# Optimization experiments

Hardware: AMD Instinct MI355X
Metric: run time of the kernel (lower is better)

Reference implementation:

```python
import jax, jax.numpy as jnp
import numpy as np

B, H, W, C = 8, 112, 112, 128
NH, WS, SR, HIDDEN = 4, 7, 8, 512
EPS = 1e-5

def ln(x, g, b):
    mu = jnp.mean(x, axis=-1, keepdims=True)
    var = jnp.var(x, axis=-1, keepdims=True)
    return (x - mu) * jax.lax.rsqrt(var + EPS) * g + b

def local_attn(x, qkv_w, qkv_b, pw, pb):
    # windowed attention: (H,W) tiled into WSxWS windows, H%WS==W%WS==0 so no pad
    Bx, N, Cx = x.shape
    hd = Cx // NH
    _h, _w = H // WS, W // WS
    xw = x.reshape(Bx, _h, WS, _w, WS, Cx).transpose(0, 1, 3, 2, 4, 5)
    xw = xw.reshape(Bx, _h * _w, WS * WS, Cx)
    qkv = (xw @ qkv_w + qkv_b).reshape(Bx, _h * _w, WS * WS, 3, NH, hd)
    qkv = qkv.transpose(3, 0, 1, 4, 2, 5)  # 3, B, nW, NH, ws2, hd
    q, k, v = qkv[0], qkv[1], qkv[2]
    attn = jax.nn.softmax((q @ jnp.swapaxes(k, -2, -1)) * (hd ** -0.5), axis=-1)
    o = (attn @ v).transpose(0, 1, 3, 2, 4).reshape(Bx, _h, _w, WS, WS, Cx)
    o = o.transpose(0, 1, 3, 2, 4, 5).reshape(Bx, N, Cx)
    return o @ pw + pb

def global_attn(x, qw, qb, kvw, kvb, srw, srb, sng, snb, pw, pb):
    Bx, N, Cx = x.shape
    hd = Cx // NH
    q = (x @ qw + qb).reshape(Bx, N, NH, hd).transpose(0, 2, 1, 3)  # B,NH,N,hd
    xi = x.reshape(Bx, H, W, Cx)
    xs = jax.lax.conv_general_dilated(xi, srw, (SR, SR), 'VALID',
                                      dimension_numbers=('NHWC', 'HWIO', 'NHWC')) + srb
    xs = ln(xs.reshape(Bx, -1, Cx), sng, snb)  # B, M, C  (M = (H/SR)*(W/SR))
    kv = (xs @ kvw + kvb).reshape(Bx, -1, 2, NH, hd)
    k = kv[:, :, 0].transpose(0, 2, 1, 3)
    v = kv[:, :, 1].transpose(0, 2, 1, 3)
    attn = jax.nn.softmax(jnp.einsum('bhnd,bhmd->bhnm', q, k) * (hd ** -0.5), axis=-1)
    o = jnp.einsum('bhnm,bhmd->bhnd', attn, v).transpose(0, 2, 1, 3).reshape(Bx, N, Cx)
    return o @ pw + pb

def mlp(x, f1w, f1b, dww, dwb, f2w, f2b):
    h = x @ f1w + f1b
    hi = h.reshape(x.shape[0], H, W, HIDDEN)
    hi = jax.lax.conv_general_dilated(hi, dww, (1, 1), 'SAME',
                                      dimension_numbers=('NHWC', 'HWIO', 'NHWC'),
                                      feature_group_count=HIDDEN) + dwb
    h = jax.nn.gelu(hi.reshape(x.shape[0], -1, HIDDEN), approximate=False)
    return h @ f2w + f2b

def reference(x, l_n1_g, l_n1_b, l_qkv_w, l_qkv_b, l_pw, l_pb, l_n2_g, l_n2_b,
              l_f1w, l_f1b, l_dww, l_dwb, l_f2w, l_f2b,
              g_n1_g, g_n1_b, g_qw, g_qb, g_kvw, g_kvb, g_srw, g_srb, g_sng, g_snb,
              g_pw, g_pb, g_n2_g, g_n2_b, g_f1w, g_f1b, g_dww, g_dwb, g_f2w, g_f2b):
    # Local-attention Block
    x = x + local_attn(ln(x, l_n1_g, l_n1_b), l_qkv_w, l_qkv_b, l_pw, l_pb)
    x = x + mlp(ln(x, l_n2_g, l_n2_b), l_f1w, l_f1b, l_dww, l_dwb, l_f2w, l_f2b)
    # Global (spatial-reduction) attention Block
    x = x + global_attn(ln(x, g_n1_g, g_n1_b), g_qw, g_qb, g_kvw, g_kvb,
                        g_srw, g_srb, g_sng, g_snb, g_pw, g_pb)
    x = x + mlp(ln(x, g_n2_g, g_n2_b), g_f1w, g_f1b, g_dww, g_dwb, g_f2w, g_f2b)
    return x

def setup_inputs() -> dict:
    key = jax.random.key(0)
    cnt = [0]
    def rn(shp, s=0.02):
        cnt[0] += 1
        return (jax.random.normal(jax.random.fold_in(key, cnt[0]), shp, dtype=jnp.float32) * s)
    z = lambda shp: jnp.zeros(shp, jnp.float32)
    o = lambda shp: jnp.ones(shp, jnp.float32)
    return {
        'x': rn((B, H * W, C), 1.0),
        'l_n1_g': o((C,)), 'l_n1_b': z((C,)),
        'l_qkv_w': rn((C, 3 * C)), 'l_qkv_b': z((3 * C,)),
        'l_pw': rn((C, C)), 'l_pb': z((C,)),
        'l_n2_g': o((C,)), 'l_n2_b': z((C,)),
        'l_f1w': rn((C, HIDDEN)), 'l_f1b': z((HIDDEN,)),
        'l_dww': rn((3, 3, 1, HIDDEN), 0.1), 'l_dwb': z((HIDDEN,)),
        'l_f2w': rn((HIDDEN, C)), 'l_f2b': z((C,)),
        'g_n1_g': o((C,)), 'g_n1_b': z((C,)),
        'g_qw': rn((C, C)), 'g_qb': z((C,)),
        'g_kvw': rn((C, 2 * C)), 'g_kvb': z((2 * C,)),
        'g_srw': rn((SR, SR, C, C), 0.02), 'g_srb': z((C,)),
        'g_sng': o((C,)), 'g_snb': z((C,)),
        'g_pw': rn((C, C)), 'g_pb': z((C,)),
        'g_n2_g': o((C,)), 'g_n2_b': z((C,)),
        'g_f1w': rn((C, HIDDEN)), 'g_f1b': z((HIDDEN,)),
        'g_dww': rn((3, 3, 1, HIDDEN), 0.1), 'g_dwb': z((HIDDEN,)),
        'g_f2w': rn((HIDDEN, C)), 'g_f2b': z((C,)),
    }
```

## Files before the change

kernel.cpp:

```cpp
#include <hip/hip_runtime.h>
#include <hip/hip_bf16.h>

#define DI __device__ __forceinline__

typedef __attribute__((ext_vector_type(8))) __bf16 bf16x8;
typedef __attribute__((ext_vector_type(8))) short short8;
typedef __attribute__((ext_vector_type(4))) short short4v;
typedef __attribute__((ext_vector_type(4))) float f32x4;
typedef __attribute__((ext_vector_type(2))) float f32x2;

DI short f2b(float f) {
    union { float f; unsigned u; } v; v.f = f;
    unsigned r = v.u + 0x7FFFu + ((v.u >> 16) & 1u);
    return (short)(r >> 16);
}
DI float b2f(short s) {
    union { unsigned u; float f; } v; v.u = ((unsigned)(unsigned short)s) << 16;
    return v.f;
}
DI float lo16(int x) {
    union { unsigned u; float f; } v; v.u = (unsigned)x << 16; return v.f;
}
DI float hi16(int x) {
    union { unsigned u; float f; } v; v.u = (unsigned)x & 0xffff0000u; return v.f;
}

DI void gll16(const short* g, short* l) {
    __builtin_amdgcn_global_load_lds(
        (const __attribute__((address_space(1))) void*)(g),
        (__attribute__((address_space(3))) void*)(l), 16, 0, 0);
}

DI float gelu(float a) {
    float t = __expf(-1.702f * a);
    return a * __builtin_amdgcn_rcpf(1.f + t);
}

template<int OB, int HB, int HR, int LNO, int FULLK>
__global__ __launch_bounds__(512)
void gemm128(const short* __restrict__ A, int lda,
             const short* __restrict__ Wt, int ldw,
             const float* __restrict__ bias,
             void* __restrict__ Cv, int ldc,
             const short* __restrict__ R, int ldr,
             const float* __restrict__ lng, const float* __restrict__ lnb,
             short* __restrict__ lnout,
             int K)
{
    __shared__ short As[16384];
    __shared__ short Bs[16384];
    const int nx = gridDim.x;
    const int total = nx * gridDim.y;
    int bid = blockIdx.x + nx * blockIdx.y;
    if ((total & 7) == 0) bid = (bid & 7) * (total >> 3) + (bid >> 3);
    const int m0 = (bid / nx) * 128, n0 = (bid % nx) * 128;
    const int tid = threadIdx.x, lane = tid & 63, w = tid >> 6;
    const int wr = w >> 2, wc = w & 3;
    const int fr = lane & 15, fg = lane >> 4;
    const int mB = wr * 64 + fr;
    const int nB = wc * 32 + fg * 4;
    const int x7 = fr & 7;

    int2 rpre[4][2];
    if (HR) {
        #pragma unroll
        for (int mi = 0; mi < 4; mi++) {
            const long long m = m0 + mB + mi * 16;
            #pragma unroll
            for (int ni = 0; ni < 2; ni++)
                rpre[mi][ni] = *(const int2*)&R[m * ldr + n0 + nB + ni * 16];
        }
    }

    f32x4 zero = {0.f, 0.f, 0.f, 0.f};
    f32x4 acc[4][2];
    #pragma unroll
    for (int i = 0; i < 4; i++)
        #pragma unroll
        for (int j = 0; j < 2; j++) acc[i][j] = zero;

    if (FULLK) {
        #pragma unroll
        for (int i = 0; i < 4; i++) {
            const int row = i * 32 + w * 4 + (lane >> 4);
            const int chunk = lane & 15;
            const int scol = (chunk ^ (row & 7)) * 8;
            short* dA = As + (i * 32 + w * 4) * 128 + lane * 8;
            short* dB = Bs + (i * 32 + w * 4) * 128 + lane * 8;
            gll16(A  + (long long)(m0 + row) * lda + scol, dA);
            gll16(Wt + (long long)(n0 + row) * ldw + scol, dB);
        }
        asm volatile("s_waitcnt vmcnt(0)" ::: "memory");
        __builtin_amdgcn_s_barrier();
        __builtin_amdgcn_s_setprio(1);
        #pragma unroll
        for (int kt = 0; kt < 4; kt++) {
            const int kc = ((kt * 4 + fg) ^ x7) * 8;
            bf16x8 af[4], bfr[2];
            #pragma unroll
            for (int mi = 0; mi < 4; mi++)
                af[mi] = *(const bf16x8*)(As + (mB + mi * 16) * 128 + kc);
            #pragma unroll
            for (int ni = 0; ni < 2; ni++)
                bfr[ni] = *(const bf16x8*)(Bs + (wc * 32 + ni * 16 + fr) * 128 + kc);
            #pragma unroll
            for (int mi = 0; mi < 4; mi++)
                #pragma unroll
                for (int ni = 0; ni < 2; ni++)
                    acc[mi][ni] = __builtin_amdgcn_mfma_f32_16x16x32_bf16(bfr[ni], af[mi], acc[mi][ni], 0, 0, 0);
        }
        __builtin_amdgcn_s_setprio(0);
    } else {
        auto STAGE = [&](int buf, int t) {
            #pragma unroll
            for (int i = 0; i < 2; i++) {
                const int row = i * 64 + w * 8 + (lane >> 3);
                const int chunk = lane & 7;
                const int scol = t * 64 + (chunk ^ (row & 7)) * 8;
                short* dA = As + buf * 8192 + (i * 64 + w * 8) * 64 + lane * 8;
                short* dB = Bs + buf * 8192 + (i * 64 + w * 8) * 64 + lane * 8;
                gll16(A  + (long long)(m0 + row) * lda + scol, dA);
                gll16(Wt + (long long)(n0 + row) * ldw + scol, dB);
            }
        };
        auto COMPUTE = [&](int buf) {
            __builtin_amdgcn_s_setprio(1);
            #pragma unroll
            for (int kt = 0; kt < 2; kt++) {
                const int kc = ((kt * 4 + fg) ^ x7) * 8;
                bf16x8 af[4], bfr[2];
                #pragma unroll
                for (int mi = 0; mi < 4; mi++)
                    af[mi] = *(const bf16x8*)(As + buf * 8192 + (mB + mi * 16) * 64 + kc);
                #pragma unroll
                for (int ni = 0; ni < 2; ni++)
                    bfr[ni] = *(const bf16x8*)(Bs + buf * 8192 + (wc * 32 + ni * 16 + fr) * 64 + kc);
                #pragma unroll
                for (int mi = 0; mi < 4; mi++)
                    #pragma unroll
                    for (int ni = 0; ni < 2; ni++)
                        acc[mi][ni] = __builtin_amdgcn_mfma_f32_16x16x32_bf16(bfr[ni], af[mi], acc[mi][ni], 0, 0, 0);
            }
            __builtin_amdgcn_s_setprio(0);
        };
        const int NT = K >> 6;
        STAGE(0, 0);
        for (int t = 0; t < NT; t++) {
            if (t + 1 < NT) {
                STAGE((t + 1) & 1, t + 1);
                asm volatile("s_waitcnt vmcnt(4)" ::: "memory");
            } else {
                asm volatile("s_waitcnt vmcnt(0)" ::: "memory");
            }
            __builtin_amdgcn_s_barrier();
            COMPUTE(t & 1);
            __builtin_amdgcn_s_barrier();
        }
    }

    if (LNO) {
        float s1[4] = {0.f, 0.f, 0.f, 0.f}, s2[4] = {0.f, 0.f, 0.f, 0.f};
        #pragma unroll
        for (int mi = 0; mi < 4; mi++) {
            const long long m = m0 + mB + mi * 16;
            #pragma unroll
            for (int ni = 0; ni < 2; ni++) {
                const int n = nB + ni * 16;
                float4 bv = *(const float4*)&bias[n];
                const float* bvp = (const float*)&bv;
                float rv[4] = {lo16(rpre[mi][ni].x), hi16(rpre[mi][ni].x),
                               lo16(rpre[mi][ni].y), hi16(rpre[mi][ni].y)};
                #pragma unroll
                for (int v = 0; v < 4; v++) {
                    float val = acc[mi][ni][v] + bvp[v] + rv[v];
                    acc[mi][ni][v] = val;
                    s1[mi] += val;
                    s2[mi] += val * val;
                }
                int2 pk;
                pk.x = ((int)(unsigned short)f2b(acc[mi][ni][1]) << 16) | (unsigned short)f2b(acc[mi][ni][0]);
                pk.y = ((int)(unsigned short)f2b(acc[mi][ni][3]) << 16) | (unsigned short)f2b(acc[mi][ni][2]);
                *(int2*)&((short*)Cv)[m * ldc + n] = pk;
            }
        }
        #pragma unroll
        for (int mi = 0; mi < 4; mi++) {
            s1[mi] += __shfl_xor(s1[mi], 16); s1[mi] += __shfl_xor(s1[mi], 32);
            s2[mi] += __shfl_xor(s2[mi], 16); s2[mi] += __shfl_xor(s2[mi], 32);
        }
        float* sc = (float*)As;
        __syncthreads();
        if (fg == 0) {
            #pragma unroll
            for (int mi = 0; mi < 4; mi++) {
                int rt = mB + mi * 16;
                sc[rt * 8 + wc * 2]     = s1[mi];
                sc[rt * 8 + wc * 2 + 1] = s2[mi];
            }
        }
        __syncthreads();
        #pragma unroll
        for (int mi = 0; mi < 4; mi++) {
            int rt = mB + mi * 16;
            long long m = m0 + rt;
            float t1 = (sc[rt * 8 + 0] + sc[rt * 8 + 2]) + (sc[rt * 8 + 4] + sc[rt * 8 + 6]);
            float t2 = (sc[rt * 8 + 1] + sc[rt * 8 + 3]) + (sc[rt * 8 + 5] + sc[rt * 8 + 7]);
            float mu = t1 * 0.0078125f;
            float var = t2 * 0.0078125f - mu * mu;
            float rs = rsqrtf(var + 1e-5f);
            #pragma unroll
            for (int ni = 0; ni < 2; ni++) {
                int n = nB + ni * 16;
                float4 gg = *(const float4*)&lng[n];
                float4 bb = *(const float4*)&lnb[n];
                const float* gp = (const float*)&gg;
                const float* bp = (const float*)&bb;
                short o[4];
                #pragma unroll
                for (int v = 0; v < 4; v++)
                    o[v] = f2b((acc[mi][ni][v] - mu) * rs * gp[v] + bp[v]);
                int2 pk;
                pk.x = ((int)(unsigned short)o[1] << 16) | (unsigned short)o[0];
                pk.y = ((int)(unsigned short)o[3] << 16) | (unsigned short)o[2];
                *(int2*)&lnout[m * 128 + n] = pk;
            }
        }
    } else {
        #pragma unroll
        for (int mi = 0; mi < 4; mi++) {
            const long long m = m0 + mB + mi * 16;
            #pragma unroll
            for (int ni = 0; ni < 2; ni++) {
                const int n = n0 + nB + ni * 16;
                float4 bv = {0.f, 0.f, 0.f, 0.f};
                if (HB) bv = *(const float4*)&bias[n];
                const float* bvp = (const float*)&bv;
                float rv[4] = {0.f, 0.f, 0.f, 0.f};
                if (HR) {
                    rv[0] = lo16(rpre[mi][ni].x); rv[1] = hi16(rpre[mi][ni].x);
                    rv[2] = lo16(rpre[mi][ni].y); rv[3] = hi16(rpre[mi][ni].y);
                }
                float val[4];
                #pragma unroll
                for (int v = 0; v < 4; v++)
                    val[v] = acc[mi][ni][v] + bvp[v] + rv[v];
                if (OB) {
                    int2 pk;
                    pk.x = ((int)(unsigned short)f2b(val[1]) << 16) | (unsigned short)f2b(val[0]);
                    pk.y = ((int)(unsigned short)f2b(val[3]) << 16) | (unsigned short)f2b(val[2]);
                    *(int2*)&((short*)Cv)[m * ldc + n] = pk;
                } else {
                    float4 st = {val[0], val[1], val[2], val[3]};
                    *(float4*)&((float*)Cv)[m * ldc + n] = st;
                }
            }
        }
    }
}

template<int OB, int HB>
__global__ __launch_bounds__(256)
void gemm64(const short* __restrict__ A, int lda, long long sA,
            const short* __restrict__ Wt, int ldw, long long sW,
            const float* __restrict__ bias,
            void* __restrict__ Cv, int ldc, long long sC,
            int M, int N, int K)
{
    __shared__ short As[2048];
    __shared__ short Bs[2048];
    const int z = blockIdx.z;
    A  += (long long)z * sA;
    Wt += (long long)z * sW;
    const int m0 = blockIdx.y * 64, n0 = blockIdx.x * 64;
    const int tid = threadIdx.x, lane = tid & 63, wv = tid >> 6;
    const int wr = wv >> 1, wc = wv & 1;
    const int lrow = tid >> 2, lch = tid & 3;
    const int wch = lch ^ (lrow & 3);

    f32x4 zero = {0.f, 0.f, 0.f, 0.f};
    f32x4 acc00 = zero, acc01 = zero, acc10 = zero, acc11 = zero;

    const short* arow = &A[(long long)(m0 + lrow) * lda + lch * 8];
    const short* brow = &Wt[(long long)(n0 + lrow) * ldw + lch * 8];
    short* asw = &As[lrow * 32 + wch * 8];
    short* bsw = &Bs[lrow * 32 + wch * 8];

    const int fr = lane & 15, fg = lane >> 4;
    const int c = ((fg ^ (fr & 3)) * 8);
    const int a0off = (wr * 32 + fr) * 32 + c;
    const int b0off = (wc * 32 + fr) * 32 + c;

    for (int k0 = 0; k0 < K; k0 += 32) {
        uint4 av = *(const uint4*)arow; arow += 32;
        uint4 bv = *(const uint4*)brow; brow += 32;
        __syncthreads();
        *(uint4*)asw = av;
        *(uint4*)bsw = bv;
        __syncthreads();
        bf16x8 a0 = *(const bf16x8*)&As[a0off];
        bf16x8 a1 = *(const bf16x8*)&As[a0off + 512];
        bf16x8 b0 = *(const bf16x8*)&Bs[b0off];
        bf16x8 b1 = *(const bf16x8*)&Bs[b0off + 512];
        acc00 = __builtin_amdgcn_mfma_f32_16x16x32_bf16(a0, b0, acc00, 0, 0, 0);
        acc01 = __builtin_amdgcn_mfma_f32_16x16x32_bf16(a0, b1, acc01, 0, 0, 0);
        acc10 = __builtin_amdgcn_mfma_f32_16x16x32_bf16(a1, b0, acc10, 0, 0, 0);
        acc11 = __builtin_amdgcn_mfma_f32_16x16x32_bf16(a1, b1, acc11, 0, 0, 0);
    }

    const long long cz = (long long)z * sC;
    const int rbase = m0 + wr * 32 + fg * 4;
    const int cbase = n0 + wc * 32 + fr;
    auto emit = [&](f32x4 a, int mi, int ni) {
        int cc = cbase + ni * 16;
        if (cc >= N) return;
        float bv = HB ? bias[cc] : 0.f;
        #pragma unroll
        for (int v = 0; v < 4; v++) {
            int rr = rbase + mi * 16 + v;
            if (rr >= M) continue;
            float val = a[v] + bv;
            if (OB) ((short*)Cv)[cz + (long long)rr * ldc + cc] = f2b(val);
            else    ((float*)Cv)[cz + (long long)rr * ldc + cc] = val;
        }
    };
    emit(acc00, 0, 0); emit(acc01, 0, 1); emit(acc10, 1, 0); emit(acc11, 1, 1);
}

__global__ __launch_bounds__(256)
void srgemm(const short* __restrict__ LNF, const short* __restrict__ Wt,
            float* __restrict__ PART)
{
    __shared__ short As[2048];
    __shared__ short Bs[2048];
    const int z = blockIdx.z;
    const int m0 = blockIdx.y * 64, n0 = blockIdx.x * 64;
    const int tid = threadIdx.x, lane = tid & 63, wv = tid >> 6;
    const int wr = wv >> 1, wc = wv & 1;
    const int lrow = tid >> 2, lch = tid & 3;
    const int wch = lch ^ (lrow & 3);

    f32x4 zero = {0.f, 0.f, 0.f, 0.f};
    f32x4 acc00 = zero, acc01 = zero, acc10 = zero, acc11 = zero;

    int row = m0 + lrow;
    int rc = row < 1568 ? row : 1567;
    int b = rc / 196, p = rc % 196;
    int oh = p / 14, ow = p % 14;
    int k0 = z * 256;
    int kh = k0 >> 10, koff = k0 & 1023;
    const short* arow = LNF + ((long long)(b * 12544 + (oh * 8 + kh) * 112 + ow * 8)) * 128
                        + koff + lch * 8;
    const short* brow = Wt + (long long)(n0 + lrow) * 8192 + k0 + lch * 8;
    short* asw = &As[lrow * 32 + wch * 8];
    short* bsw = &Bs[lrow * 32 + wch * 8];

    const int fr = lane & 15, fg = lane >> 4;
    const int c = ((fg ^ (fr & 3)) * 8);
    const int a0off = (wr * 32 + fr) * 32 + c;
    const int b0off = (wc * 32 + fr) * 32 + c;

    for (int kk = 0; kk < 256; kk += 32) {
        uint4 av = *(const uint4*)arow; arow += 32;
        uint4 bv = *(const uint4*)brow; brow += 32;
        __syncthreads();
        *(uint4*)asw = av;
        *(uint4*)bsw = bv;
        __syncthreads();
        bf16x8 a0 = *(const bf16x8*)&As[a0off];
        bf16x8 a1 = *(const bf16x8*)&As[a0off + 512];
        bf16x8 b0 = *(const bf16x8*)&Bs[b0off];
        bf16x8 b1 = *(const bf16x8*)&Bs[b0off + 512];
        acc00 = __builtin_amdgcn_mfma_f32_16x16x32_bf16(a0, b0, acc00, 0, 0, 0);
        acc01 = __builtin_amdgcn_mfma_f32_16x16x32_bf16(a0, b1, acc01, 0, 0, 0);
        acc10 = __builtin_amdgcn_mfma_f32_16x16x32_bf16(a1, b0, acc10, 0, 0, 0);
        acc11 = __builtin_amdgcn_mfma_f32_16x16x32_bf16(a1, b1, acc11, 0, 0, 0);
    }

    const int rbase = m0 + wr * 32 + fg * 4;
    const int cbase = n0 + wc * 32 + fr;
    auto emit = [&](f32x4 a, int mi, int ni) {
        int cc = cbase + ni * 16;
        #pragma unroll
        for (int v = 0; v < 4; v++) {
            int rr = rbase + mi * 16 + v;
            if (rr >= 1568) continue;
            PART[(long long)z * 200704 + (long long)rr * 128 + cc] = a[v];
        }
    };
    emit(acc00, 0, 0); emit(acc01, 0, 1); emit(acc10, 1, 0); emit(acc11, 1, 1);
}

__global__ void reduceXS(const float* __restrict__ PART, const float* __restrict__ bias,
                         float* __restrict__ XS)
{
    int i = blockIdx.x * 256 + threadIdx.x;
    float s = 0.f;
    #pragma unroll
    for (int z = 0; z < 32; z++) s += PART[(long long)z * 200704 + i];
    XS[i] = s + bias[i & 127];
}

__global__ __launch_bounds__(256)
void ln_kernel(const float* __restrict__ x, const float* __restrict__ g,
               const float* __restrict__ b, short* __restrict__ o, int rows)
{
    int row = blockIdx.x * 4 + (threadIdx.x >> 6);
    if (row >= rows) return;
    int lane = threadIdx.x & 63;
    const float2 v = *(const float2*)&x[(long long)row * 128 + lane * 2];
    float s = v.x + v.y;
    float ss = v.x * v.x + v.y * v.y;
    #pragma unroll
    for (int off = 1; off < 64; off <<= 1) {
        s += __shfl_xor(s, off);
        ss += __shfl_xor(ss, off);
    }
    float mu = s * 0.0078125f;
    float var = ss * 0.0078125f - mu * mu;
    float rs = rsqrtf(var + 1e-5f);
    float2 gg = *(const float2*)&g[lane * 2];
    float2 bb = *(const float2*)&b[lane * 2];
    short2 out;
    out.x = f2b((v.x - mu) * rs * gg.x + bb.x);
    out.y = f2b((v.y - mu) * rs * gg.y + bb.y);
    *(short2*)&o[(long long)row * 128 + lane * 2] = out;
}

__global__ __launch_bounds__(256)
void ln_first(const float* __restrict__ x, const float* __restrict__ g,
              const float* __restrict__ b, short* __restrict__ o,
              short* __restrict__ res)
{
    int row = blockIdx.x * 4 + (threadIdx.x >> 6);
    int lane = threadIdx.x & 63;
    const float2 v = *(const float2*)&x[(long long)row * 128 + lane * 2];
    short2 rc;
    rc.x = f2b(v.x); rc.y = f2b(v.y);
    *(short2*)&res[(long long)row * 128 + lane * 2] = rc;
    float s = v.x + v.y;
    float ss = v.x * v.x + v.y * v.y;
    #pragma unroll
    for (int off = 1; off < 64; off <<= 1) {
        s += __shfl_xor(s, off);
        ss += __shfl_xor(ss, off);
    }
    float mu = s * 0.0078125f;
    float var = ss * 0.0078125f - mu * mu;
    float rs = rsqrtf(var + 1e-5f);
    float2 gg = *(const float2*)&g[lane * 2];
    float2 bb = *(const float2*)&b[lane * 2];
    short2 out;
    out.x = f2b((v.x - mu) * rs * gg.x + bb.x);
    out.y = f2b((v.y - mu) * rs * gg.y + bb.y);
    *(short2*)&o[(long long)row * 128 + lane * 2] = out;
}

__global__ void wtrans(const float* __restrict__ w, short* __restrict__ wt, int K, int N)
{
    long long idx = (long long)blockIdx.x * 256 + threadIdx.x;
    if (idx >= (long long)K * N) return;
    int k = (int)(idx / N), n = (int)(idx % N);
    wt[(long long)n * K + k] = f2b(w[idx]);
}

__global__ void packkv(const short* __restrict__ kvb, short* __restrict__ kp,
                       short* __restrict__ vt)
{
    int idx = blockIdx.x * 256 + threadIdx.x;
    if (idx >= 229376) return;
    int d = idx & 31;
    int m = (idx >> 5) % 224;
    int bh = idx / (224 * 32);
    int b = bh >> 2, h = bh & 3;
    short kv = 0, vv = 0;
    if (m < 196) {
        long long src = ((long long)b * 196 + m) * 256 + h * 32 + d;
        kv = kvb[src];
        vv = kvb[src + 128];
    }
    if (m < 208) kp[((long long)bh * 208 + m) * 32 + d] = kv;
    vt[((long long)bh * 32 + d) * 224 + m] = vv;
}

__global__ __launch_bounds__(512)
void lattn(const short* __restrict__ qkv, short* __restrict__ att)
{
    __shared__ short QKs[64 * 264];
    __shared__ short Vt[128 * 72];
    __shared__ short Pl[8 * 16 * 72];
    const int bi = blockIdx.x >> 8;
    const int win = blockIdx.x & 255;
    const int wy = win >> 4, wx = win & 15;
    const long long base = (long long)bi * 12544;
    const int tid = threadIdx.x;

    for (int i = tid; i < 1152; i += 512) {
        uint4 zz = {0, 0, 0, 0};
        *(uint4*)&Vt[i * 8] = zz;
    }
    __syncthreads();

    for (int idx = tid; idx < 2352; idx += 512) {
        int i = idx / 48, ch = idx % 48;
        long long n = base + (wy * 7 + i / 7) * 112 + wx * 7 + i % 7;
        uint4 v = *(const uint4*)&qkv[n * 384 + ch * 8];
        if (ch < 32) {
            *(uint4*)&QKs[i * 264 + ch * 8] = v;
        } else {
            int c0 = (ch - 32) * 8;
            const short* sp = (const short*)&v;
            #pragma unroll
            for (int u = 0; u < 8; u++) {
                int cc = c0 + u;
                Vt[cc * 72 + ((((i >> 3) ^ ((cc >> 3) & 7)) << 3) | (i & 7))] = sp[u];
            }
        }
    }
    __syncthreads();

    const int w = tid >> 6, l = tid & 63;
    const int h = w >> 1, qh = w & 1;
    const int q16 = l & 15, g = l >> 4;
    const float SC = 0.17677669529663689f;
    f32x4 zero = {0.f, 0.f, 0.f, 0.f};

    bf16x8 kf[4];
    #pragma unroll
    for (int kt = 0; kt < 4; kt++)
        kf[kt] = *(const bf16x8*)&QKs[(kt * 16 + q16) * 264 + 128 + h * 32 + g * 8];
    bf16x8 vf[2][2];
    #pragma unroll
    for (int dt = 0; dt < 2; dt++) {
        int cc = h * 32 + dt * 16 + q16;
        #pragma unroll
        for (int s2 = 0; s2 < 2; s2++)
            vf[dt][s2] = *(const bf16x8*)&Vt[cc * 72 + (((s2 * 4 + g) ^ ((cc >> 3) & 7)) << 3)];
    }
    short* pw = &Pl[(w * 16 + q16) * 72];

    for (int qt2 = 0; qt2 < 2; qt2++) {
        int qt = qh * 2 + qt2;
        bf16x8 qf = *(const bf16x8*)&QKs[(qt * 16 + q16) * 264 + h * 32 + g * 8];
        f32x4 s[4];
        #pragma unroll
        for (int kt = 0; kt < 4; kt++)
            s[kt] = __builtin_amdgcn_mfma_f32_16x16x32_bf16(kf[kt], qf, zero, 0, 0, 0);
        float mx = -1e30f;
        #pragma unroll
        for (int kt = 0; kt < 4; kt++) {
            #pragma unroll
            for (int v = 0; v < 4; v++) {
                int k = kt * 16 + g * 4 + v;
                if (k < 49) mx = fmaxf(mx, s[kt][v]);
            }
        }
        mx = fmaxf(mx, __shfl_xor(mx, 16));
        mx = fmaxf(mx, __shfl_xor(mx, 32));
        float sum = 0.f;
        #pragma unroll
        for (int kt = 0; kt < 4; kt++) {
            #pragma unroll
            for (int v = 0; v < 4; v++) {
                int k = kt * 16 + g * 4 + v;
                float p = (k < 49) ? __expf(SC * (s[kt][v] - mx)) : 0.f;
                s[kt][v] = p;
                sum += p;
            }
        }
        sum += __shfl_xor(sum, 16);
        sum += __shfl_xor(sum, 32);
        float inv = 1.f / sum;
        #pragma unroll
        for (int kt = 0; kt < 4; kt++) {
            int lo = ((int)(unsigned short)f2b(s[kt][1] * inv) << 16) | (unsigned short)f2b(s[kt][0] * inv);
            int hi = ((int)(unsigned short)f2b(s[kt][3] * inv) << 16) | (unsigned short)f2b(s[kt][2] * inv);
            int2 pr; pr.x = lo; pr.y = hi;
            *(int2*)&pw[kt * 16 + g * 4] = pr;
        }
        f32x4 o0 = zero, o1 = zero;
        #pragma unroll
        for (int s2 = 0; s2 < 2; s2++) {
            bf16x8 pa = *(const bf16x8*)&pw[s2 * 32 + g * 8];
            o0 = __builtin_amdgcn_mfma_f32_16x16x32_bf16(pa, vf[0][s2], o0, 0, 0, 0);
            o1 = __builtin_amdgcn_mfma_f32_16x16x32_bf16(pa, vf[1][s2], o1, 0, 0, 0);
        }
        #pragma unroll
        for (int v = 0; v < 4; v++) {
            int q = qt * 16 + g * 4 + v;
            if (q < 49) {
                long long n = base + (wy * 7 + q / 7) * 112 + wx * 7 + q % 7;
                att[n * 128 + h * 32 + q16]      = f2b(o0[v]);
                att[n * 128 + h * 32 + 16 + q16] = f2b(o1[v]);
            }
        }
    }
}

__global__ __launch_bounds__(256)
void gattn(const short* __restrict__ Q, const short* __restrict__ KP,
           const short* __restrict__ VT, short* __restrict__ O)
{
    __shared__ short Ks[208 * 40];
    __shared__ short Vt[32 * 232];
    __shared__ short Pl[4 * 16 * 136];
    const int qb = blockIdx.x;
    const int bh = blockIdx.y;
    const int b = bh >> 2, h = bh & 3;
    const int tid = threadIdx.x, w = tid >> 6, l = tid & 63;
    const int q16 = l & 15, g = l >> 4;

    for (int idx = tid; idx < 832; idx += 256) {
        int m = idx >> 2, dg = idx & 3;
        uint4 v = *(const uint4*)&KP[((long long)bh * 208 + m) * 32 + dg * 8];
        *(uint4*)&Ks[m * 40 + ((dg ^ (m & 3)) * 8)] = v;
    }
    for (int idx = tid; idx < 896; idx += 256) {
        int d = idx / 28, mg = idx % 28;
        uint4 v = *(const uint4*)&VT[((long long)bh * 32 + d) * 224 + mg * 8];
        *(uint4*)&Vt[d * 232 + mg * 8] = v;
    }
    const long long qbase = (long long)b * 12544 + qb * 128 + w * 32;
    bf16x8 qfa = *(const bf16x8*)&Q[(qbase + q16) * 128 + h * 32 + g * 8];
    bf16x8 qfb = *(const bf16x8*)&Q[(qbase + 16 + q16) * 128 + h * 32 + g * 8];
    __syncthreads();

    const float SC = 0.17677669529663689f;
    f32x4 zero = {0.f, 0.f, 0.f, 0.f};
    short* pw = &Pl[(w * 16 + q16) * 136];
    const int xk = (g ^ (q16 & 3)) * 8;

    #pragma unroll
    for (int qt = 0; qt < 2; qt++) {
        bf16x8 qf = qt ? qfb : qfa;
        f32x4 s[13];
        #pragma unroll
        for (int t = 0; t < 13; t++) {
            bf16x8 a = *(const bf16x8*)&Ks[(t * 16 + q16) * 40 + xk];
            s[t] = __builtin_amdgcn_mfma_f32_16x16x32_bf16(a, qf, zero, 0, 0, 0);
        }
        float sum = 0.f;
        #pragma unroll
        for (int t = 0; t < 8; t++) {
            float p0 = __expf(SC * s[t][0]);
            float p1 = __expf(SC * s[t][1]);
            float p2 = __expf(SC * s[t][2]);
            float p3 = __expf(SC * s[t][3]);
            sum += (p0 + p1) + (p2 + p3);
            int2 pr;
            pr.x = ((int)(unsigned short)f2b(p1) << 16) | (unsigned short)f2b(p0);
            pr.y = ((int)(unsigned short)f2b(p3) << 16) | (unsigned short)f2b(p2);
            *(int2*)&pw[t * 16 + g * 4] = pr;
        }
        f32x4 o0 = zero, o1 = zero;
        #pragma unroll
        for (int kc = 0; kc < 4; kc++) {
            bf16x8 pa = *(const bf16x8*)&pw[kc * 32 + g * 8];
            bf16x8 v0 = *(const bf16x8*)&Vt[q16 * 232 + kc * 32 + g * 8];
            bf16x8 v1 = *(const bf16x8*)&Vt[(16 + q16) * 232 + kc * 32 + g * 8];
            o0 = __builtin_amdgcn_mfma_f32_16x16x32_bf16(v0, pa, o0, 0, 0, 0);
            o1 = __builtin_amdgcn_mfma_f32_16x16x32_bf16(v1, pa, o1, 0, 0, 0);
        }
        #pragma unroll
        for (int t = 8; t < 13; t++) {
            float p[4];
            #pragma unroll
            for (int v = 0; v < 4; v++) {
                int k = t * 16 + g * 4 + v;
                p[v] = (k < 196) ? __expf(SC * s[t][v]) : 0.f;
                sum += p[v];
            }
            int2 pr;
            pr.x = ((int)(unsigned short)f2b(p[1]) << 16) | (unsigned short)f2b(p[0]);
            pr.y = ((int)(unsigned short)f2b(p[3]) << 16) | (unsigned short)f2b(p[2]);
            *(int2*)&pw[(t - 8) * 16 + g * 4] = pr;
        }
        {
            int2 zz; zz.x = 0; zz.y = 0;
            *(int2*)&pw[80 + g * 4] = zz;
        }
        sum += __shfl_xor(sum, 16);
        sum += __shfl_xor(sum, 32);
        #pragma unroll
        for (int kc = 0; kc < 3; kc++) {
            bf16x8 pa = *(const bf16x8*)&pw[kc * 32 + g * 8];
            bf16x8 v0 = *(const bf16x8*)&Vt[q16 * 232 + 128 + kc * 32 + g * 8];
            bf16x8 v1 = *(const bf16x8*)&Vt[(16 + q16) * 232 + 128 + kc * 32 + g * 8];
            o0 = __builtin_amdgcn_mfma_f32_16x16x32_bf16(v0, pa, o0, 0, 0, 0);
            o1 = __builtin_amdgcn_mfma_f32_16x16x32_bf16(v1, pa, o1, 0, 0, 0);
        }
        const float inv = 1.f / sum;
        const long long r = qbase + qt * 16 + q16;
        int2 p0, p1;
        p0.x = ((int)(unsigned short)f2b(o0[1] * inv) << 16) | (unsigned short)f2b(o0[0] * inv);
        p0.y = ((int)(unsigned short)f2b(o0[3] * inv) << 16) | (unsigned short)f2b(o0[2] * inv);
        p1.x = ((int)(unsigned short)f2b(o1[1] * inv) << 16) | (unsigned short)f2b(o1[0] * inv);
        p1.y = ((int)(unsigned short)f2b(o1[3] * inv) << 16) | (unsigned short)f2b(o1[2] * inv);
        *(int2*)&O[r * 128 + h * 32 + g * 4]      = p0;
        *(int2*)&O[r * 128 + h * 32 + 16 + g * 4] = p1;
    }
}

__global__ __launch_bounds__(256)
void dwgelu(const short* __restrict__ h1, const float* __restrict__ w,
            const float* __restrict__ bias, short* __restrict__ h2)
{
    int bid = blockIdx.x;
    bid = (bid & 7) * (gridDim.x >> 3) + (bid >> 3);
    const int idx = bid * 256 + threadIdx.x;
    const int cg = idx & 127;
    const int rem = idx >> 7;
    const int img = rem / 1568;
    const int t = rem % 1568;
    const int x0 = (t % 56) * 2;
    const int y0 = (t / 56) * 4;
    const int c0 = cg << 2;

    f32x2 wreg[9][2];
    #pragma unroll
    for (int tp = 0; tp < 9; tp++) {
        float4 v = *(const float4*)&w[tp * 512 + c0];
        wreg[tp][0][0] = v.x; wreg[tp][0][1] = v.y;
        wreg[tp][1][0] = v.z; wreg[tp][1][1] = v.w;
    }
    float4 bv = *(const float4*)&bias[c0];
    f32x2 acc[4][2][2];
    #pragma unroll
    for (int r = 0; r < 4; r++)
        #pragma unroll
        for (int oc = 0; oc < 2; oc++) {
            acc[r][oc][0][0] = bv.x; acc[r][oc][0][1] = bv.y;
            acc[r][oc][1][0] = bv.z; acc[r][oc][1][1] = bv.w;
        }
    const long long ibase = (long long)img * 12544;

    if (x0 >= 1 && x0 <= 109 && y0 >= 1 && y0 <= 107) {
        const short* base = &h1[(ibase + (long long)(y0 - 1) * 112 + (x0 - 1)) * 512 + c0];
        #pragma unroll
        for (int dy = 0; dy < 6; dy++) {
            f32x2 rowf[4][2];
            #pragma unroll
            for (int kx = 0; kx < 4; kx++) {
                short4v sv = *(const short4v*)&base[((long long)dy * 112 + kx) * 512];
                rowf[kx][0][0] = b2f(sv[0]); rowf[kx][0][1] = b2f(sv[1]);
                rowf[kx][1][0] = b2f(sv[2]); rowf[kx][1][1] = b2f(sv[3]);
            }
            #pragma unroll
            for (int ky = 0; ky < 3; ky++) {
                const int r = dy - ky;
                if (r < 0 || r > 3) continue;
                #pragma unroll
                for (int oc = 0; oc < 2; oc++)
                    #pragma unroll
                    for (int kx = 0; kx < 3; kx++) {
                        acc[r][oc][0] = __builtin_elementwise_fma(rowf[oc + kx][0], wreg[ky * 3 + kx][0], acc[r][oc][0]);
                        acc[r][oc][1] = __builtin_elementwise_fma(rowf[oc + kx][1], wreg[ky * 3 + kx][1], acc[r][oc][1]);
                    }
            }
        }
    } else {
        #pragma unroll
        for (int dy = -1; dy <= 4; dy++) {
            const int yy = y0 + dy;
            const bool rowok = (unsigned)yy < 112u;
            f32x2 rowf[4][2];
            #pragma unroll
            for (int kx = 0; kx < 4; kx++) {
                const int xx = x0 - 1 + kx;
                short4v sv = {0, 0, 0, 0};
                if (rowok && (unsigned)xx < 112u)
                    sv = *(const short4v*)&h1[(ibase + yy * 112 + xx) * 512 + c0];
                rowf[kx][0][0] = b2f(sv[0]); rowf[kx][0][1] = b2f(sv[1]);
                rowf[kx][1][0] = b2f(sv[2]); rowf[kx][1][1] = b2f(sv[3]);
            }
            #pragma unroll
            for (int ky = 0; ky < 3; ky++) {
                const int r = dy + 1 - ky;
                if (r < 0 || r > 3) continue;
                #pragma unroll
                for (int oc = 0; oc < 2; oc++)
                    #pragma unroll
                    for (int kx = 0; kx < 3; kx++) {
                        acc[r][oc][0] = __builtin_elementwise_fma(rowf[oc + kx][0], wreg[ky * 3 + kx][0], acc[r][oc][0]);
                        acc[r][oc][1] = __builtin_elementwise_fma(rowf[oc + kx][1], wreg[ky * 3 + kx][1], acc[r][oc][1]);
                    }
            }
        }
    }
    #pragma unroll
    for (int r = 0; r < 4; r++)
        #pragma unroll
        for (int oc = 0; oc < 2; oc++) {
            short o[4];
            o[0] = f2b(gelu(acc[r][oc][0][0]));
            o[1] = f2b(gelu(acc[r][oc][0][1]));
            o[2] = f2b(gelu(acc[r][oc][1][0]));
            o[3] = f2b(gelu(acc[r][oc][1][1]));
            int2 pk;
            pk.x = ((int)(unsigned short)o[1] << 16) | (unsigned short)o[0];
            pk.y = ((int)(unsigned short)o[3] << 16) | (unsigned short)o[2];
            *(int2*)&h2[(ibase + (y0 + r) * 112 + x0 + oc) * 512 + c0] = pk;
        }
}

extern "C" void kernel_launch(void* const* d_in, const int* in_sizes, int n_in,
                              void* d_out, int out_size, void* d_ws, size_t ws_size,
                              hipStream_t stream)
{
    (void)in_sizes; (void)n_in; (void)out_size;
    const float* X      = (const float*)d_in[0];
    const float* l_n1_g = (const float*)d_in[1];
    const float* l_n1_b = (const float*)d_in[2];
    const float* l_qkv_w= (const float*)d_in[3];
    const float* l_qkv_b= (const float*)d_in[4];
    const float* l_pw   = (const float*)d_in[5];
    const float* l_pb   = (const float*)d_in[6];
    const float* l_n2_g = (const float*)d_in[7];
    const float* l_n2_b = (const float*)d_in[8];
    const float* l_f1w  = (const float*)d_in[9];
    const float* l_f1b  = (const float*)d_in[10];
    const float* l_dww  = (const float*)d_in[11];
    const float* l_dwb  = (const float*)d_in[12];
    const float* l_f2w  = (const float*)d_in[13];
    const float* l_f2b  = (const float*)d_in[14];
    const float* g_n1_g = (const float*)d_in[15];
    const float* g_n1_b = (const float*)d_in[16];
    const float* g_qw   = (const float*)d_in[17];
    const float* g_qb   = (const float*)d_in[18];
    const float* g_kvw  = (const float*)d_in[19];
    const float* g_kvb  = (const float*)d_in[20];
    const float* g_srw  = (const float*)d_in[21];
    const float* g_srb  = (const float*)d_in[22];
    const float* g_sng  = (const float*)d_in[23];
    const float* g_snb  = (const float*)d_in[24];
    const float* g_pw   = (const float*)d_in[25];
    const float* g_pb   = (const float*)d_in[26];
    const float* g_n2_g = (const float*)d_in[27];
    const float* g_n2_b = (const float*)d_in[28];
    const float* g_f1w  = (const float*)d_in[29];
    const float* g_f1b  = (const float*)d_in[30];
    const float* g_dww  = (const float*)d_in[31];
    const float* g_dwb  = (const float*)d_in[32];
    const float* g_f2w  = (const float*)d_in[33];
    const float* g_f2b  = (const float*)d_in[34];

    const long long NPB = 12544;
    const long long BN  = 100352;

    float* OUT = (float*)d_out;
    char* ws = (char*)d_ws;
    size_t off = 0;
    auto alloc = [&](size_t bytes) { size_t o = off; off += (bytes + 255) & ~(size_t)255; return o; };
    short* WT_QKV = (short*)(ws + alloc(384 * 128 * 2));
    short* WT_LPW = (short*)(ws + alloc(128 * 128 * 2));
    short* WT_LF1 = (short*)(ws + alloc(512 * 128 * 2));
    short* WT_LF2 = (short*)(ws + alloc(128 * 512 * 2));
    short* WT_GQ  = (short*)(ws + alloc(128 * 128 * 2));
    short* WT_GKV = (short*)(ws + alloc(256 * 128 * 2));
    short* WT_GSR = (short*)(ws + alloc(128 * 8192 * 2));
    short* WT_GPW = (short*)(ws + alloc(128 * 128 * 2));
    short* WT_GF1 = (short*)(ws + alloc(512 * 128 * 2));
    short* WT_GF2 = (short*)(ws + alloc(128 * 512 * 2));
    short* LNF    = (short*)(ws + alloc((size_t)BN * 128 * 2));
    short* RES    = (short*)(ws + alloc((size_t)BN * 128 * 2));
    char*  U      = ws + alloc(0);

    const size_t SZ_H1   = (size_t)BN * 512 * 2;
    const bool big = ws_size >= off + 2 * SZ_H1 + 4096;
    short* QKVB = (short*)(U + 0);
    short* ATT  = (short*)(U + 77070336);
    float* PART = (float*)(U + 0);
    float* XS   = (float*)(U + 25690368);
    short* XSLN = (short*)(U + 26493184);
    short* KVB  = (short*)(U + 26894592);
    short* QBUF = (short*)(U + 27697408);
    short* KP   = (short*)(U + 53387776);
    short* VT   = (short*)(U + 53387776 + 425984);

    wtrans<<<192, 256, 0, stream>>>(l_qkv_w, WT_QKV, 128, 384);
    wtrans<<<64, 256, 0, stream>>>(l_pw, WT_LPW, 128, 128);
    wtrans<<<256, 256, 0, stream>>>(l_f1w, WT_LF1, 128, 512);
    wtrans<<<256, 256, 0, stream>>>(l_f2w, WT_LF2, 512, 128);
    wtrans<<<64, 256, 0, stream>>>(g_qw, WT_GQ, 128, 128);
    wtrans<<<128, 256, 0, stream>>>(g_kvw, WT_GKV, 128, 256);
    wtrans<<<4096, 256, 0, stream>>>(g_srw, WT_GSR, 8192, 128);
    wtrans<<<64, 256, 0, stream>>>(g_pw, WT_GPW, 128, 128);
    wtrans<<<256, 256, 0, stream>>>(g_f1w, WT_GF1, 128, 512);
    wtrans<<<256, 256, 0, stream>>>(g_f2w, WT_GF2, 512, 128);

    const int CB = big ? 8 : 2;
    short* H1 = (short*)(U + 0);

    ln_first<<<25088, 256, 0, stream>>>(X, l_n1_g, l_n1_b, LNF, RES);
    gemm128<1, 1, 0, 0, 1><<<dim3(3, 784), 512, 0, stream>>>(
        LNF, 128, WT_QKV, 128, l_qkv_b, QKVB, 384, nullptr, 0,
        nullptr, nullptr, nullptr, 128);
    lattn<<<2048, 512, 0, stream>>>(QKVB, ATT);
    gemm128<1, 1, 1, 1, 1><<<dim3(1, 784), 512, 0, stream>>>(
        ATT, 128, WT_LPW, 128, l_pb, RES, 128, RES, 128,
        l_n2_g, l_n2_b, LNF, 128);

    {
        short* H2 = (short*)(U + (size_t)CB * NPB * 512 * 2);
        for (int b0 = 0; b0 < 8; b0 += CB) {
            int Mc = CB * 12544;
            gemm128<1, 1, 0, 0, 1><<<dim3(4, Mc / 128), 512, 0, stream>>>(
                LNF + (long long)b0 * NPB * 128, 128, WT_LF1, 128, l_f1b,
                H1, 512, nullptr, 0, nullptr, nullptr, nullptr, 128);
            dwgelu<<<CB * 784, 256, 0, stream>>>(H1, l_dww, l_dwb, H2);
            gemm128<1, 1, 1, 1, 0><<<dim3(1, Mc / 128), 512, 0, stream>>>(
                H2, 512, WT_LF2, 512, l_f2b,
                RES + (long long)b0 * NPB * 128, 128,
                RES + (long long)b0 * NPB * 128, 128,
                g_n1_g, g_n1_b, LNF + (long long)b0 * NPB * 128, 512);
        }
    }

    gemm128<1, 1, 0, 0, 1><<<dim3(1, 784), 512, 0, stream>>>(
        LNF, 128, WT_GQ, 128, g_qb, QBUF, 128, nullptr, 0,
        nullptr, nullptr, nullptr, 128);
    srgemm<<<dim3(2, 25, 32), 256, 0, stream>>>(LNF, WT_GSR, PART);
    reduceXS<<<784, 256, 0, stream>>>(PART, g_srb, XS);
    ln_kernel<<<392, 256, 0, stream>>>(XS, g_sng, g_snb, XSLN, 1568);
    gemm64<1, 1><<<dim3(4, 25, 1), 256, 0, stream>>>(
        XSLN, 128, 0, WT_GKV, 128, 0, g_kvb,
        KVB, 256, 0, 1568, 256, 128);
    packkv<<<896, 256, 0, stream>>>(KVB, KP, VT);
    gattn<<<dim3(98, 32), 256, 0, stream>>>(QBUF, KP, VT, ATT);
    gemm128<1, 1, 1, 1, 1><<<dim3(1, 784), 512, 0, stream>>>(
        ATT, 128, WT_GPW, 128, g_pb, RES, 128, RES, 128,
        g_n2_g, g_n2_b, LNF, 128);

    {
        short* H2 = (short*)(U + (size_t)CB * NPB * 512 * 2);
        for (int b0 = 0; b0 < 8; b0 += CB) {
            int Mc = CB * 12544;
            gemm128<1, 1, 0, 0, 1><<<dim3(4, Mc / 128), 512, 0, stream>>>(
                LNF + (long long)b0 * NPB * 128, 128, WT_GF1, 128, g_f1b,
                H1, 512, nullptr, 0, nullptr, nullptr, nullptr, 128);
            dwgelu<<<CB * 784, 256, 0, stream>>>(H1, g_dww, g_dwb, H2);
            gemm128<0, 1, 1, 0, 0><<<dim3(1, Mc / 128), 512, 0, stream>>>(
                H2, 512, WT_GF2, 512, g_f2b,
                OUT + (long long)b0 * NPB * 128, 128,
                RES + (long long)b0 * NPB * 128, 128,
                nullptr, nullptr, nullptr, 512);
        }
    }
}
```

Measured before the change: 542.3 us.

## Switch GEMMs to 256x128 tiles with 1024 threads and K=32 double-buffered staging

Replaces the 128x128 GEMM (512 threads, either full-K single-shot or 64-wide K double buffering) with a 256x128 tile computed by 16 waves, each still owning a 64x32 output sub-tile. K is staged in 32-wide double-buffered slices with a 4-chunk XOR swizzle, which halves the B-tile shared memory and shares each weight tile across twice as many rows. The aim is more weight reuse per block and a single pipelined path for all K. The cost is more loop iterations and barriers per K, with 1024-thread barriers, and half as many blocks in flight. The epilogue was not shown being updated for 16 waves, so it is unclear whether it handles wr up to 3 correctly.

```diff
diff --git a/kernel.cpp b/kernel.cpp
--- a/kernel.cpp
+++ b/kernel.cpp
@@ -36,9 +36,9 @@
     return a * __builtin_amdgcn_rcpf(1.f + t);
 }
 
-template<int OB, int HB, int HR, int LNO, int FULLK>
-__global__ __launch_bounds__(512)
-void gemm128(const short* __restrict__ A, int lda,
+template<int OB, int HB, int HR, int LNO>
+__global__ __launch_bounds__(1024)
+void gemm256(const short* __restrict__ A, int lda,
              const short* __restrict__ Wt, int ldw,
              const float* __restrict__ bias,
              void* __restrict__ Cv, int ldc,
@@ -48,18 +48,22 @@
              int K)
 {
     __shared__ short As[16384];
-    __shared__ short Bs[16384];
+    __shared__ short Bs[8192];
     const int nx = gridDim.x;
     const int total = nx * gridDim.y;
     int bid = blockIdx.x + nx * blockIdx.y;
     if ((total & 7) == 0) bid = (bid & 7) * (total >> 3) + (bid >> 3);
-    const int m0 = (bid / nx) * 128, n0 = (bid % nx) * 128;
+    const int m0 = (bid / nx) * 256, n0 = (bid % nx) * 128;
     const int tid = threadIdx.x, lane = tid & 63, w = tid >> 6;
     const int wr = w >> 2, wc = w & 3;
     const int fr = lane & 15, fg = lane >> 4;
     const int mB = wr * 64 + fr;
     const int nB = wc * 32 + fg * 4;
-    const int x7 = fr & 7;
+
+    const int ar = tid >> 2, ap = tid & 3;
+    const int br = ar & 127;
+    const int ascol = (ap ^ (ar & 3)) * 8;
+    const int bscol = (ap ^ (br & 3)) * 8;
 
     int2 rpre[4][2];
     if (HR) {
@@ -79,83 +83,42 @@
         #pragma unroll
         for (int j = 0; j < 2; j++) acc[i][j] = zero;
 
-    if (FULLK) {
-        #pragma unroll
-        for (int i = 0; i < 4; i++) {
-            const int row = i * 32 + w * 4 + (lane >> 4);
-            const int chunk = lane & 15;
-            const int scol = (chunk ^ (row & 7)) * 8;
-            short* dA = As + (i * 32 + w * 4) * 128 + lane * 8;
-            short* dB = Bs + (i * 32 + w * 4) * 128 + lane * 8;
-            gll16(A  + (long long)(m0 + row) * lda + scol, dA);
-            gll16(Wt + (long long)(n0 + row) * ldw + scol, dB);
-        }
-        asm volatile("s_waitcnt vmcnt(0)" ::: "memory");
+    auto STAGE = [&](int buf, int t) {
+        gll16(A  + (long long)(m0 + ar) * lda + t * 32 + ascol,
+              As + buf * 8192 + tid * 8);
+        gll16(Wt + (long long)(n0 + br) * ldw + t * 32 + bscol,
+              Bs + buf * 4096 + ((tid * 8) & 4095));
+    };
+    auto COMPUTE = [&](int buf) {
+        const int kc = (fg ^ (fr & 3)) * 8;
+        bf16x8 af[4], bfr[2];
+        #pragma unroll
+        for (int mi = 0; mi < 4; mi++)
+            af[mi] = *(const bf16x8*)(As + buf * 8192 + (mB + mi * 16) * 32 + kc);
+        #pragma unroll
+        for (int ni = 0; ni < 2; ni++)
+            bfr[ni] = *(const bf16x8*)(Bs + buf * 4096 + (wc * 32 + ni * 16 + fr) * 32 + kc);
+        __builtin_amdgcn_s_setprio(1);
+        #pragma unroll
+        for (int mi = 0; mi < 4; mi++)
+            #pragma unroll
+            for (int ni = 0; ni < 2; ni++)
+                acc[mi][ni] = __builtin_amdgcn_mfma_f32_16x16x32_bf16(bfr[ni], af[mi], acc[mi][ni], 0, 0, 0);
+        __builtin_amdgcn_s_setprio(0);
+    };
+
+    const int NT = K >> 5;
+    STAGE(0, 0);
+    for (int t = 0; t < NT; t++) {
+        if (t + 1 < NT) {
+            STAGE((t + 1) & 1, t + 1);
+            asm volatile("s_waitcnt vmcnt(2)" ::: "memory");
+        } else {
+            asm volatile("s_waitcnt vmcnt(0)" ::: "memory");
+        }
         __builtin_amdgcn_s_barrier();
-        __builtin_amdgcn_s_setprio(1);
-        #pragma unroll
-        for (int kt = 0; kt < 4; kt++) {
-            const int kc = ((kt * 4 + fg) ^ x7) * 8;
-            bf16x8 af[4], bfr[2];
-            #pragma unroll
-            for (int mi = 0; mi < 4; mi++)
-                af[mi] = *(const bf16x8*)(As + (mB + mi * 16) * 128 + kc);
-            #pragma unroll
-            for (int ni = 0; ni < 2; ni++)
-                bfr[ni] = *(const bf16x8*)(Bs + (wc * 32 + ni * 16 + fr) * 128 + kc);
-            #pragma unroll
-            for (int mi = 0; mi < 4; mi++)
-                #pragma unroll
-                for (int ni = 0; ni < 2; ni++)
-                    acc[mi][ni] = __builtin_amdgcn_mfma_f32_16x16x32_bf16(bfr[ni], af[mi], acc[mi][ni], 0, 0, 0);
-        }
-        __builtin_amdgcn_s_setprio(0);
-    } else {
-        auto STAGE = [&](int buf, int t) {
-            #pragma unroll
-            for (int i = 0; i < 2; i++) {
-                const int row = i * 64 + w * 8 + (lane >> 3);
-                const int chunk = lane & 7;
-                const int scol = t * 64 + (chunk ^ (row & 7)) * 8;
-                short* dA = As + buf * 8192 + (i * 64 + w * 8) * 64 + lane * 8;
-                short* dB = Bs + buf * 8192 + (i * 64 + w * 8) * 64 + lane * 8;
-                gll16(A  + (long long)(m0 + row) * lda + scol, dA);
-                gll16(Wt + (long long)(n0 + row) * ldw + scol, dB);
-            }
-        };
-        auto COMPUTE = [&](int buf) {
-            __builtin_amdgcn_s_setprio(1);
-            #pragma unroll
-            for (int kt = 0; kt < 2; kt++) {
-                const int kc = ((kt * 4 + fg) ^ x7) * 8;
-                bf16x8 af[4], bfr[2];
-                #pragma unroll
-                for (int mi = 0; mi < 4; mi++)
-                    af[mi] = *(const bf16x8*)(As + buf * 8192 + (mB + mi * 16) * 64 + kc);
-                #pragma unroll
-                for (int ni = 0; ni < 2; ni++)
-                    bfr[ni] = *(const bf16x8*)(Bs + buf * 8192 + (wc * 32 + ni * 16 + fr) * 64 + kc);
-                #pragma unroll
-                for (int mi = 0; mi < 4; mi++)
-                    #pragma unroll
-                    for (int ni = 0; ni < 2; ni++)
-                        acc[mi][ni] = __builtin_amdgcn_mfma_f32_16x16x32_bf16(bfr[ni], af[mi], acc[mi][ni], 0, 0, 0);
-            }
-            __builtin_amdgcn_s_setprio(0);
-        };
-        const int NT = K >> 6;
-        STAGE(0, 0);
-        for (int t = 0; t < NT; t++) {
-            if (t + 1 < NT) {
-                STAGE((t + 1) & 1, t + 1);
-                asm volatile("s_waitcnt vmcnt(4)" ::: "memory");
-            } else {
-                asm volatile("s_waitcnt vmcnt(0)" ::: "memory");
-            }
-            __builtin_amdgcn_s_barrier();
-            COMPUTE(t & 1);
-            __builtin_amdgcn_s_barrier();
-        }
+        COMPUTE(t & 1);
+        __builtin_amdgcn_s_barrier();
     }
 
     if (LNO) {
@@ -891,11 +854,11 @@
     short* H1 = (short*)(U + 0);
 
     ln_first<<<25088, 256, 0, stream>>>(X, l_n1_g, l_n1_b, LNF, RES);
-    gemm128<1, 1, 0, 0, 1><<<dim3(3, 784), 512, 0, stream>>>(
+    gemm256<1, 1, 0, 0><<<dim3(3, 392), 1024, 0, stream>>>(
         LNF, 128, WT_QKV, 128, l_qkv_b, QKVB, 384, nullptr, 0,
         nullptr, nullptr, nullptr, 128);
     lattn<<<2048, 512, 0, stream>>>(QKVB, ATT);
-    gemm128<1, 1, 1, 1, 1><<<dim3(1, 784), 512, 0, stream>>>(
+    gemm256<1, 1, 1, 1><<<dim3(1, 392), 1024, 0, stream>>>(
         ATT, 128, WT_LPW, 128, l_pb, RES, 128, RES, 128,
         l_n2_g, l_n2_b, LNF, 128);
 
@@ -903,11 +866,11 @@
         short* H2 = (short*)(U + (size_t)CB * NPB * 512 * 2);
         for (int b0 = 0; b0 < 8; b0 += CB) {
             int Mc = CB * 12544;
-            gemm128<1, 1, 0, 0, 1><<<dim3(4, Mc / 128), 512, 0, stream>>>(
+            gemm256<1, 1, 0, 0><<<dim3(4, Mc / 256), 1024, 0, stream>>>(
                 LNF + (long long)b0 * NPB * 128, 128, WT_LF1, 128, l_f1b,
                 H1, 512, nullptr, 0, nullptr, nullptr, nullptr, 128);
             dwgelu<<<CB * 784, 256, 0, stream>>>(H1, l_dww, l_dwb, H2);
-            gemm128<1, 1, 1, 1, 0><<<dim3(1, Mc / 128), 512, 0, stream>>>(
+            gemm256<1, 1, 1, 1><<<dim3(1, Mc / 256), 1024, 0, stream>>>(
                 H2, 512, WT_LF2, 512, l_f2b,
                 RES + (long long)b0 * NPB * 128, 128,
                 RES + (long long)b0 * NPB * 128, 128,
@@ -915,7 +878,7 @@
         }
     }
 
-    gemm128<1, 1, 0, 0, 1><<<dim3(1, 784), 512, 0, stream>>>(
+    gemm256<1, 1, 0, 0><<<dim3(1, 392), 1024, 0, stream>>>(
         LNF, 128, WT_GQ, 128, g_qb, QBUF, 128, nullptr, 0,
         nullptr, nullptr, nullptr, 128);
     srgemm<<<dim3(2, 25, 32), 256, 0, stream>>>(LNF, WT_GSR, PART);
@@ -926,7 +889,7 @@
         KVB, 256, 0, 1568, 256, 128);
     packkv<<<896, 256, 0, stream>>>(KVB, KP, VT);
     gattn<<<dim3(98, 32), 256, 0, stream>>>(QBUF, KP, VT, ATT);
-    gemm128<1, 1, 1, 1, 1><<<dim3(1, 784), 512, 0, stream>>>(
+    gemm256<1, 1, 1, 1><<<dim3(1, 392), 1024, 0, stream>>>(
         ATT, 128, WT_GPW, 128, g_pb, RES, 128, RES, 128,
         g_n2_g, g_n2_b, LNF, 128);
 
@@ -934,11 +897,11 @@
         short* H2 = (short*)(U + (size_t)CB * NPB * 512 * 2);
         for (int b0 = 0; b0 < 8; b0 += CB) {
             int Mc = CB * 12544;
-            gemm128<1, 1, 0, 0, 1><<<dim3(4, Mc / 128), 512, 0, stream>>>(
+            gemm256<1, 1, 0, 0><<<dim3(4, Mc / 256), 1024, 0, stream>>>(
                 LNF + (long long)b0 * NPB * 128, 128, WT_GF1, 128, g_f1b,
                 H1, 512, nullptr, 0, nullptr, nullptr, nullptr, 128);
             dwgelu<<<CB * 784, 256, 0, stream>>>(H1, g_dww, g_dwb, H2);
-            gemm128<0, 1, 1, 0, 0><<<dim3(1, Mc / 128), 512, 0, stream>>>(
+            gemm256<0, 1, 1, 0><<<dim3(1, Mc / 256), 1024, 0, stream>>>(
                 H2, 512, WT_GF2, 512, g_f2b,
                 OUT + (long long)b0 * NPB * 128, 128,
                 RES + (long long)b0 * NPB * 128, 128,
```

Result: slower. 597.7 us (+10.2%).
